# Performance work log

Measured on AMD Instinct MI355X. Metric: run time of the kernel, lower is better.

The kernel has to match this reference:

```python
import jax, jax.numpy as jnp
import numpy as np
import math

IN_C, OUT_C, KH, KW = 128, 128, 3, 3
GROUPS_NUM, NUM_W = 8, 8
STRIDE, PAD, DIL = 1, 1, 1
BETA = 1.0


def setup_inputs() -> dict:
    key = jax.random.key(0)
    ks = jax.random.split(key, 6)
    B, H, W = 8, 56, 56
    n = IN_C * KH * KW
    bound = math.sqrt(6.0 / n)  # reset_parameters bound for weight templates
    inputs = jax.random.normal(ks[0], (B, IN_C, H, W), jnp.float32)
    mask = jax.random.randint(ks[1], (B, H, W), 0, GROUPS_NUM)
    Alpha = jax.random.uniform(ks[2], (B, GROUPS_NUM, H, W), jnp.float32)
    weight_templates = jax.random.uniform(ks[3], (OUT_C * IN_C * KH * KW, NUM_W), jnp.float32, -bound, bound)
    routing_w = jax.random.normal(ks[4], (GROUPS_NUM * NUM_W, IN_C), jnp.float32) * 0.01
    routing_b = jnp.zeros((GROUPS_NUM * NUM_W,), jnp.float32)
    bias = jnp.zeros((OUT_C,), jnp.float32)
    return dict(inputs=inputs, mask=mask, Alpha=Alpha, weight_templates=weight_templates,
                routing_w=routing_w, routing_b=routing_b, bias=bias, use_alpha=1)


def _unfold(x):
    # torch F.unfold-compatible im2col: [B, C*KH*KW, Ho, Wo], channel-major feature order
    return jax.lax.conv_general_dilated_patches(
        x, (KH, KW), (STRIDE, STRIDE), [(PAD, PAD), (PAD, PAD)],
        rhs_dilation=(DIL, DIL), dimension_numbers=('NCHW', 'OIHW', 'NCHW'))


def reference(inputs, mask, Alpha, weight_templates, routing_w, routing_b, bias, use_alpha):
    B, C, H, W = inputs.shape
    K = IN_C * KH * KW
    # SE-style routing: GAP -> fc -> scaled sigmoid (alpha=1.0 in source)
    x_se = inputs.reshape(B, C, -1).mean(-1)                              # [B, C]
    x_se = 2.0 * jax.nn.sigmoid(x_se @ routing_w.T + routing_b) / NUM_W   # [B, G*num_W]
    # blend weight templates: F.linear(x_se.reshape(-1,num_W), weight)
    w = x_se.reshape(B * GROUPS_NUM, NUM_W) @ weight_templates.T          # [B*G, O*K]
    w = w.reshape(B, GROUPS_NUM, OUT_C, K).transpose(0, 2, 3, 1)          # [B, O, K, G]
    patches = _unfold(inputs)                                             # [B, K, Ho, Wo]
    # per-group convolution outputs, then per-pixel group routing
    y = jnp.einsum('bokg,bkhw->boghw', w, patches)                        # [B, O, G, Ho, Wo]
    if use_alpha:
        probs = jax.nn.softmax(BETA * Alpha, axis=1)                      # soft routing [B, G, Ho, Wo]
    else:
        probs = jax.nn.one_hot(mask, GROUPS_NUM, axis=1, dtype=y.dtype)   # hard per-pixel group select
    out = jnp.einsum('boghw,bghw->bohw', y, probs)
    return out + bias.reshape(1, -1, 1, 1)
```

## Files before the change

### kernel.cpp

```cpp
#include <hip/hip_runtime.h>
#include <stdint.h>

#define IN_C   128
#define OUT_C  128
#define KTOT   1152
#define NG     8
#define NW     8
#define NB     8
#define HH     56
#define WWID   56
#define NPIX   3136
#define PPAD   3200
#define MTOT   1024
#define HALO   58
#define HPIX   (HALO*HALO)


typedef __attribute__((ext_vector_type(8))) short short8;
typedef __attribute__((ext_vector_type(8))) unsigned short ushort8;
typedef __attribute__((ext_vector_type(4))) float f32x4;

__device__ __forceinline__ unsigned short f2bf(float f) {
    unsigned u = __float_as_uint(f);
    u += 0x7FFF + ((u >> 16) & 1);
    return (unsigned short)(u >> 16);
}

__device__ __forceinline__ void cp16(const unsigned short* g, unsigned short* l) {
    __builtin_amdgcn_global_load_lds(
        (const __attribute__((address_space(1))) unsigned int*)g,
        (__attribute__((address_space(3))) unsigned int*)l,
        16, 0, 0);
}

__global__ __launch_bounds__(256) void prep_kernel(const float* __restrict__ in,
                                                   const float* __restrict__ T,
                                                   float* __restrict__ xse,
                                                   unsigned short* __restrict__ Apack,
                                                   unsigned short* __restrict__ Xt) {
    __shared__ __align__(16) unsigned char smem[32768];
    const int blk = blockIdx.x;
    const int t = threadIdx.x;

    if (blk < 1024) {
        const float* src = in + (size_t)blk * NPIX;
        float s = 0.f;
        for (int i = t; i < NPIX / 4; i += 256) {
            float4 v = ((const float4*)src)[i];
            s += v.x + v.y + v.z + v.w;
        }
        #pragma unroll
        for (int off = 32; off; off >>= 1) s += __shfl_down(s, off);
        float* ws4 = (float*)smem;
        if ((t & 63) == 0) ws4[t >> 6] = s;
        __syncthreads();
        if (t == 0)
            xse[blk] = (ws4[0] + ws4[1] + ws4[2] + ws4[3]) * (1.0f / (float)NPIX);
        return;
    }
    if (blk < 1152) {
        unsigned short* lh = (unsigned short*)smem;
        const int o = blk - 1024;
        const float* To = T + (size_t)o * 9216;
        #pragma unroll
        for (int it = 0; it < 9; it++) {
            const int f = it * 256 + t;
            const float4 v = ((const float4*)To)[f];
            ushort4 h;
            h.x = f2bf(v.x); h.y = f2bf(v.y); h.z = f2bf(v.z); h.w = f2bf(v.w);
            *(ushort4*)&lh[f * 4] = h;
        }
        __syncthreads();
        const int m16b = o >> 1;
        const int lrb = (o & 1) * 8;
        #pragma unroll
        for (int it = 0; it < 5; it++) {
            const int ch = it * 256 + t;
            if (ch < 1152) {
                const int j = ch & 7, kc = ch >> 3;
                const int s = kc >> 4, c0 = (kc & 15) << 3;
                const int kt = kc >> 2, lq = kc & 3;
                ushort8 v;
                #pragma unroll
                for (int i = 0; i < 8; i++)
                    v[i] = lh[((c0 + i) * 9 + s) * 8 + j];
                const size_t off = ((((size_t)m16b * 36 + kt) * 4 + lq) * 16 + lrb + j) * 8;
                *(ushort8*)&Apack[off] = v;
            }
        }
        return;
    }
    unsigned short* tile = (unsigned short*)smem;
    const int idx = blk - 1152;
    const int yt = idx % 28;
    const int b  = idx / 28;
    const int y0 = yt * 2;

    #pragma unroll
    for (int it = 0; it < 14; it++) {
        const int f = it * 256 + t;
        const int c = f / 28;
        const int rem = f - c * 28;
        const int y = rem / 14;
        const int x4 = rem - y * 14;
        const float4 v = *(const float4*)(in + ((size_t)(b * IN_C + c)) * NPIX
                                          + (y0 + y) * WWID + x4 * 4);
        unsigned short bf0 = f2bf(v.x), bf1 = f2bf(v.y), bf2 = f2bf(v.z), bf3 = f2bf(v.w);
        const int ppb = (y * WWID + x4 * 4) ^ (((c >> 3) & 15) << 2);
        uint2 pk;
        pk.x = (unsigned)bf0 | ((unsigned)bf1 << 16);
        pk.y = (unsigned)bf2 | ((unsigned)bf3 << 16);
        *(uint2*)&tile[c * 128 + ppb] = pk;
    }
    __syncthreads();

    #pragma unroll
    for (int it = 0; it < 7; it++) {
        const int ch = it * 256 + t;
        const int oct = ch & 15;
        const int pp = ch >> 4;
        const int sw = oct << 2;
        ushort8 v;
        #pragma unroll
        for (int i = 0; i < 8; i++)
            v[i] = tile[(oct * 8 + i) * 128 + (pp ^ sw)];
        const int y2 = (pp >= WWID) ? 1 : 0;
        const int xg = pp - y2 * WWID;
        const size_t hp = (size_t)b * HPIX + (y0 + y2 + 1) * HALO + (xg + 1);
        *(ushort8*)&Xt[hp * 128 + oct * 8] = v;
    }

    if (t < 64) {
        const int pi = t >> 4, oct = t & 15;
        const int yy = y0 + 1 + (pi >> 1);
        const int xx = (pi & 1) * 57;
        *(ushort8*)&Xt[((size_t)b * HPIX + yy * HALO + xx) * 128 + oct * 8] =
            (ushort8){0, 0, 0, 0, 0, 0, 0, 0};
    }
    if (yt == 0 || yt == 27) {
        const int yy = (yt == 0) ? 0 : 57;
        #pragma unroll
        for (int it = 0; it < 4; it++) {
            const int ch = it * 256 + t;
            if (ch < 928) {
                const int xx = ch >> 4, oct = ch & 15;
                *(ushort8*)&Xt[((size_t)b * HPIX + yy * HALO + xx) * 128 + oct * 8] =
                    (ushort8){0, 0, 0, 0, 0, 0, 0, 0};
            }
        }
    }
}

__global__ __launch_bounds__(256) void s_kernel(const float* __restrict__ Alpha,
                                                const int* __restrict__ mask,
                                                const float* __restrict__ xse,
                                                const float* __restrict__ rw,
                                                const float* __restrict__ rb,
                                                const int* __restrict__ use_alpha,
                                                float* __restrict__ Sws) {
    const int b = blockIdx.y;
    const int t = threadIdx.x;
    const int p = blockIdx.x * 256 + t;
    __shared__ float xs[IN_C];
    __shared__ float rsh[64];
    if (t < IN_C) xs[t] = xse[b * IN_C + t];
    __syncthreads();
    if (t < 64) {
        float acc = rb[t];
        #pragma unroll 8
        for (int c = 0; c < IN_C; c++) acc += xs[c] * rw[t * IN_C + c];
        rsh[t] = 0.25f / (1.0f + expf(-acc));
    }
    __syncthreads();
    if (p >= PPAD) return;
    float sj[8] = {0, 0, 0, 0, 0, 0, 0, 0};
    if (p < NPIX) {
        float pr[8];
        if (use_alpha[0]) {
            float a[8], m = -1e30f;
            #pragma unroll
            for (int g = 0; g < 8; g++) {
                a[g] = Alpha[((size_t)(b * NG + g)) * NPIX + p];
                m = fmaxf(m, a[g]);
            }
            float sum = 0.f;
            #pragma unroll
            for (int g = 0; g < 8; g++) { pr[g] = expf(a[g] - m); sum += pr[g]; }
            float inv = 1.f / sum;
            #pragma unroll
            for (int g = 0; g < 8; g++) pr[g] *= inv;
        } else {
            int mg = mask[(size_t)b * NPIX + p];
            #pragma unroll
            for (int g = 0; g < 8; g++) pr[g] = (g == mg) ? 1.f : 0.f;
        }
        #pragma unroll
        for (int g = 0; g < 8; g++)
            #pragma unroll
            for (int j = 0; j < 8; j++) sj[j] += pr[g] * rsh[g * 8 + j];
    }
    float* dst = Sws + ((size_t)b * PPAD + p) * 8;
    *(f32x4*)dst = (f32x4){sj[0], sj[1], sj[2], sj[3]};
    *(f32x4*)(dst + 4) = (f32x4){sj[4], sj[5], sj[6], sj[7]};
}

__global__ __launch_bounds__(256) void gemm_kernel(const unsigned short* __restrict__ Apack,
                                                   const unsigned short* __restrict__ Xt,
                                                   const float* __restrict__ Sws,
                                                   const float* __restrict__ bias,
                                                   float* __restrict__ out) {
    __shared__ __align__(16) unsigned short Bsh[4][512 * 8];
    const int tid = threadIdx.x;
    const int wv = tid >> 6, ln = tid & 63;
    const int lq = ln >> 4, lr = ln & 15;
    const int wrow = wv >> 1, wcol = wv & 1;

    const int lid = blockIdx.x;
    const int b   = lid & 7;
    const int sl  = lid >> 3;
    const int mt  = sl & 7;
    const int nt  = sl >> 3;

    f32x4 acc[4][4];
    #pragma unroll
    for (int i = 0; i < 4; i++)
        #pragma unroll
        for (int j = 0; j < 4; j++) acc[i][j] = (f32x4){0.f, 0.f, 0.f, 0.f};

    const int js = tid & 3;
    const int r0 = tid >> 2,  q0 = js ^ (r0 & 3) ^ ((r0 >> 2) & 3);
    const int r1 = r0 + 64,   q1 = js ^ (r1 & 3) ^ ((r1 >> 2) & 3);
    const int p0 = min(nt * 128 + r0, NPIX - 1);
    const int p1 = min(nt * 128 + r1, NPIX - 1);
    const int y0p = p0 / WWID, x0p = p0 - y0p * WWID;
    const int y1p = p1 / WWID, x1p = p1 - y1p * WWID;
    const unsigned short* gb0 = Xt + ((size_t)b * HPIX + y0p * HALO + x0p) * 128 + q0 * 8;
    const unsigned short* gb1 = Xt + ((size_t)b * HPIX + y1p * HALO + x1p) * 128 + q1 * 8;
    unsigned short* lbA[4];
    #pragma unroll
    for (int i = 0; i < 4; i++) lbA[i] = &Bsh[i][(wv * 64) * 8];

    const unsigned short* gaw[4];
    #pragma unroll
    for (int tm = 0; tm < 4; tm++) {
        const int m16 = mt * 8 + wrow * 4 + tm;
        gaw[tm] = Apack + ((size_t)m16 * 36 * 64 + ln) * 8;
    }

    const int jj = lq ^ (lr & 3) ^ ((lr >> 2) & 3);

    cp16(gb0, lbA[0]); cp16(gb1, lbA[0] + 256 * 8);
    cp16(gb0 + 32, lbA[1]); cp16(gb1 + 32, lbA[1] + 256 * 8);
    short8 af[2][4];
    #pragma unroll
    for (int tm = 0; tm < 4; tm++) af[0][tm] = *(const short8*)(gaw[tm]);
    #pragma unroll
    for (int tm = 0; tm < 4; tm++) af[1][tm] = *(const short8*)(gaw[tm] + 512);

    #pragma unroll 1
    for (int pr = 0; pr < 18; pr++) {
        __syncthreads();
        const int st2 = pr * 2 + 2, st3 = pr * 2 + 3;
        if (pr < 17) {
            const int nk2 = st2 * 32, s2 = nk2 >> 7;
            const int kh2 = s2 / 3, kw2 = s2 - 3 * kh2;
            const int off2 = (kh2 * HALO + kw2) * 128 + (nk2 & 127);
            const int nk3 = st3 * 32, s3 = nk3 >> 7;
            const int kh3 = s3 / 3, kw3 = s3 - 3 * kh3;
            const int off3 = (kh3 * HALO + kw3) * 128 + (nk3 & 127);
            unsigned short* d2 = lbA[st2 & 3];
            unsigned short* d3 = lbA[st3 & 3];
            cp16(gb0 + off2, d2); cp16(gb1 + off2, d2 + 256 * 8);
            cp16(gb0 + off3, d3); cp16(gb1 + off3, d3 + 256 * 8);
        }
        const int bufa = (pr & 1) * 2;
        {
            short8 bfr[4];
            #pragma unroll
            for (int tn = 0; tn < 4; tn++) {
                const int row = wcol * 64 + tn * 16 + lr;
                bfr[tn] = *(const short8*)&Bsh[bufa][(row * 4 + jj) * 8];
            }
            #pragma unroll
            for (int tm = 0; tm < 4; tm++)
                #pragma unroll
                for (int tn = 0; tn < 4; tn++)
                    acc[tm][tn] = __builtin_amdgcn_mfma_f32_16x16x32_bf16(
                        af[0][tm], bfr[tn], acc[tm][tn], 0, 0, 0);
        }
        if (pr < 17) {
            #pragma unroll
            for (int tm = 0; tm < 4; tm++)
                af[0][tm] = *(const short8*)(gaw[tm] + (size_t)st2 * 512);
        }
        {
            short8 bfr[4];
            #pragma unroll
            for (int tn = 0; tn < 4; tn++) {
                const int row = wcol * 64 + tn * 16 + lr;
                bfr[tn] = *(const short8*)&Bsh[bufa + 1][(row * 4 + jj) * 8];
            }
            #pragma unroll
            for (int tm = 0; tm < 4; tm++)
                #pragma unroll
                for (int tn = 0; tn < 4; tn++)
                    acc[tm][tn] = __builtin_amdgcn_mfma_f32_16x16x32_bf16(
                        af[1][tm], bfr[tn], acc[tm][tn], 0, 0, 0);
        }
        if (pr < 17) {
            #pragma unroll
            for (int tm = 0; tm < 4; tm++)
                af[1][tm] = *(const short8*)(gaw[tm] + (size_t)st3 * 512);
        }
    }

    const int j0 = (lq & 1) * 4;
    const int oo = lq >> 1;
    #pragma unroll
    for (int tm = 0; tm < 4; tm++) {
        const int o = mt * 16 + wrow * 8 + tm * 2 + oo;
        const float bo = bias[o];
        #pragma unroll
        for (int tn = 0; tn < 4; tn++) {
            const int p = nt * 128 + wcol * 64 + tn * 16 + lr;
            const f32x4 sv = *(const f32x4*)&Sws[((size_t)b * PPAD + p) * 8 + j0];
            const f32x4 a = acc[tm][tn];
            float part = a.x * sv.x + a.y * sv.y + a.z * sv.z + a.w * sv.w;
            float tot = part + __shfl_xor(part, 16);
            if ((lq & 1) == 0 && p < NPIX)
                out[((size_t)b * OUT_C + o) * NPIX + p] = tot + bo;
        }
    }
}

extern "C" void kernel_launch(void* const* d_in, const int* in_sizes, int n_in,
                              void* d_out, int out_size, void* d_ws, size_t ws_size,
                              hipStream_t stream) {
    const float* inputs = (const float*)d_in[0];
    const int*   mask   = (const int*)d_in[1];
    const float* Alpha  = (const float*)d_in[2];
    const float* wtmpl  = (const float*)d_in[3];
    const float* rw     = (const float*)d_in[4];
    const float* rb     = (const float*)d_in[5];
    const float* bias   = (const float*)d_in[6];
    const int*   ua     = (const int*)d_in[7];
    float* out = (float*)d_out;

    char* ws = (char*)d_ws;
    unsigned short* Xt  = (unsigned short*)ws;
    unsigned short* Apk = (unsigned short*)(ws + 6889472);
    float*          Sws = (float*)(ws + 9248768);
    float*          xse = (float*)(ws + 10067968);

    prep_kernel<<<1376, 256, 0, stream>>>(inputs, wtmpl, xse, Apk, Xt);
    s_kernel<<<dim3(13, NB), 256, 0, stream>>>(Alpha, mask, xse, rw, rb, ua, Sws);
    gemm_kernel<<<1600, 256, 0, stream>>>(Apk, Xt, Sws, bias, out);
}
```

Baseline: 162.8 us.

## Interleave async LDS copies with MFMA clusters using barriers and priority

```diff
diff --git a/kernel.cpp b/kernel.cpp
--- a/kernel.cpp
+++ b/kernel.cpp
@@ -248,70 +248,107 @@
     }
 
     const int jj = lq ^ (lr & 3) ^ ((lr >> 2) & 3);
+    const int rowb = wcol * 64 + lr;
 
     cp16(gb0, lbA[0]); cp16(gb1, lbA[0] + 256 * 8);
     cp16(gb0 + 32, lbA[1]); cp16(gb1 + 32, lbA[1] + 256 * 8);
+    __builtin_amdgcn_sched_barrier(0);
     short8 af[2][4];
     #pragma unroll
     for (int tm = 0; tm < 4; tm++) af[0][tm] = *(const short8*)(gaw[tm]);
     #pragma unroll
     for (int tm = 0; tm < 4; tm++) af[1][tm] = *(const short8*)(gaw[tm] + 512);
+    __builtin_amdgcn_sched_barrier(0);
 
     #pragma unroll 1
     for (int pr = 0; pr < 18; pr++) {
-        __syncthreads();
         const int st2 = pr * 2 + 2, st3 = pr * 2 + 3;
-        if (pr < 17) {
-            const int nk2 = st2 * 32, s2 = nk2 >> 7;
-            const int kh2 = s2 / 3, kw2 = s2 - 3 * kh2;
-            const int off2 = (kh2 * HALO + kw2) * 128 + (nk2 & 127);
-            const int nk3 = st3 * 32, s3 = nk3 >> 7;
-            const int kh3 = s3 / 3, kw3 = s3 - 3 * kh3;
-            const int off3 = (kh3 * HALO + kw3) * 128 + (nk3 & 127);
-            unsigned short* d2 = lbA[st2 & 3];
-            unsigned short* d3 = lbA[st3 & 3];
-            cp16(gb0 + off2, d2); cp16(gb1 + off2, d2 + 256 * 8);
-            cp16(gb0 + off3, d3); cp16(gb1 + off3, d3 + 256 * 8);
-        }
         const int bufa = (pr & 1) * 2;
+        const int nk2 = st2 * 32, s2 = nk2 >> 7;
+        const int kh2 = s2 / 3, kw2 = s2 - 3 * kh2;
+        const int off2 = (kh2 * HALO + kw2) * 128 + (nk2 & 127);
+        const int nk3 = st3 * 32, s3 = nk3 >> 7;
+        const int kh3 = s3 / 3, kw3 = s3 - 3 * kh3;
+        const int off3 = (kh3 * HALO + kw3) * 128 + (nk3 & 127);
+        unsigned short* d2 = lbA[st2 & 3];
+        unsigned short* d3 = lbA[st3 & 3];
+
+        asm volatile("s_waitcnt vmcnt(4)" ::: "memory");
+        __builtin_amdgcn_sched_barrier(0);
+        __builtin_amdgcn_s_barrier();
+
+        if (pr < 17) cp16(gb0 + off2, d2);
+        __builtin_amdgcn_sched_barrier(0);
         {
-            short8 bfr[4];
-            #pragma unroll
-            for (int tn = 0; tn < 4; tn++) {
-                const int row = wcol * 64 + tn * 16 + lr;
-                bfr[tn] = *(const short8*)&Bsh[bufa][(row * 4 + jj) * 8];
-            }
-            #pragma unroll
-            for (int tm = 0; tm < 4; tm++)
-                #pragma unroll
-                for (int tn = 0; tn < 4; tn++)
-                    acc[tm][tn] = __builtin_amdgcn_mfma_f32_16x16x32_bf16(
-                        af[0][tm], bfr[tn], acc[tm][tn], 0, 0, 0);
-        }
+            short8 bf0 = *(const short8*)&Bsh[bufa][((rowb +  0) * 4 + jj) * 8];
+            short8 bf1 = *(const short8*)&Bsh[bufa][((rowb + 16) * 4 + jj) * 8];
+            __builtin_amdgcn_s_barrier();
+            __builtin_amdgcn_s_setprio(1);
+            #pragma unroll
+            for (int tm = 0; tm < 4; tm++) {
+                acc[tm][0] = __builtin_amdgcn_mfma_f32_16x16x32_bf16(af[0][tm], bf0, acc[tm][0], 0, 0, 0);
+                acc[tm][1] = __builtin_amdgcn_mfma_f32_16x16x32_bf16(af[0][tm], bf1, acc[tm][1], 0, 0, 0);
+            }
+            __builtin_amdgcn_s_setprio(0);
+            __builtin_amdgcn_s_barrier();
+        }
+
+        if (pr < 17) cp16(gb1 + off2, d2 + 256 * 8);
+        __builtin_amdgcn_sched_barrier(0);
+        {
+            short8 bf2 = *(const short8*)&Bsh[bufa][((rowb + 32) * 4 + jj) * 8];
+            short8 bf3 = *(const short8*)&Bsh[bufa][((rowb + 48) * 4 + jj) * 8];
+            __builtin_amdgcn_s_barrier();
+            __builtin_amdgcn_s_setprio(1);
+            #pragma unroll
+            for (int tm = 0; tm < 4; tm++) {
+                acc[tm][2] = __builtin_amdgcn_mfma_f32_16x16x32_bf16(af[0][tm], bf2, acc[tm][2], 0, 0, 0);
+                acc[tm][3] = __builtin_amdgcn_mfma_f32_16x16x32_bf16(af[0][tm], bf3, acc[tm][3], 0, 0, 0);
+            }
+            __builtin_amdgcn_s_setprio(0);
+            __builtin_amdgcn_s_barrier();
+        }
+
         if (pr < 17) {
             #pragma unroll
             for (int tm = 0; tm < 4; tm++)
                 af[0][tm] = *(const short8*)(gaw[tm] + (size_t)st2 * 512);
-        }
+            cp16(gb0 + off3, d3);
+            cp16(gb1 + off3, d3 + 256 * 8);
+        }
+        __builtin_amdgcn_sched_barrier(0);
         {
-            short8 bfr[4];
-            #pragma unroll
-            for (int tn = 0; tn < 4; tn++) {
-                const int row = wcol * 64 + tn * 16 + lr;
-                bfr[tn] = *(const short8*)&Bsh[bufa + 1][(row * 4 + jj) * 8];
-            }
-            #pragma unroll
-            for (int tm = 0; tm < 4; tm++)
-                #pragma unroll
-                for (int tn = 0; tn < 4; tn++)
-                    acc[tm][tn] = __builtin_amdgcn_mfma_f32_16x16x32_bf16(
-                        af[1][tm], bfr[tn], acc[tm][tn], 0, 0, 0);
+            short8 bf0 = *(const short8*)&Bsh[bufa + 1][((rowb +  0) * 4 + jj) * 8];
+            short8 bf1 = *(const short8*)&Bsh[bufa + 1][((rowb + 16) * 4 + jj) * 8];
+            __builtin_amdgcn_s_barrier();
+            __builtin_amdgcn_s_setprio(1);
+            #pragma unroll
+            for (int tm = 0; tm < 4; tm++) {
+                acc[tm][0] = __builtin_amdgcn_mfma_f32_16x16x32_bf16(af[1][tm], bf0, acc[tm][0], 0, 0, 0);
+                acc[tm][1] = __builtin_amdgcn_mfma_f32_16x16x32_bf16(af[1][tm], bf1, acc[tm][1], 0, 0, 0);
+            }
+            __builtin_amdgcn_s_setprio(0);
+            __builtin_amdgcn_s_barrier();
+        }
+
+        {
+            short8 bf2 = *(const short8*)&Bsh[bufa + 1][((rowb + 32) * 4 + jj) * 8];
+            short8 bf3 = *(const short8*)&Bsh[bufa + 1][((rowb + 48) * 4 + jj) * 8];
+            __builtin_amdgcn_s_barrier();
+            __builtin_amdgcn_s_setprio(1);
+            #pragma unroll
+            for (int tm = 0; tm < 4; tm++) {
+                acc[tm][2] = __builtin_amdgcn_mfma_f32_16x16x32_bf16(af[1][tm], bf2, acc[tm][2], 0, 0, 0);
+                acc[tm][3] = __builtin_amdgcn_mfma_f32_16x16x32_bf16(af[1][tm], bf3, acc[tm][3], 0, 0, 0);
+            }
+            __builtin_amdgcn_s_setprio(0);
         }
         if (pr < 17) {
             #pragma unroll
             for (int tm = 0; tm < 4; tm++)
                 af[1][tm] = *(const short8*)(gaw[tm] + (size_t)st3 * 512);
         }
+        __builtin_amdgcn_sched_barrier(0);
     }
 
     const int j0 = (lq & 1) * 4;
```

New measurement: 178.1 us. 9.4% more time.

## Load B fragments directly from global into registers, drop LDS staging and barriers

Applied to the files above, without the earlier changes.

```diff
diff --git a/kernel.cpp b/kernel.cpp
--- a/kernel.cpp
+++ b/kernel.cpp
@@ -209,7 +209,6 @@
                                                    const float* __restrict__ Sws,
                                                    const float* __restrict__ bias,
                                                    float* __restrict__ out) {
-    __shared__ __align__(16) unsigned short Bsh[4][512 * 8];
     const int tid = threadIdx.x;
     const int wv = tid >> 6, ln = tid & 63;
     const int lq = ln >> 4, lr = ln & 15;
@@ -227,92 +226,57 @@
         #pragma unroll
         for (int j = 0; j < 4; j++) acc[i][j] = (f32x4){0.f, 0.f, 0.f, 0.f};
 
-    const int js = tid & 3;
-    const int r0 = tid >> 2,  q0 = js ^ (r0 & 3) ^ ((r0 >> 2) & 3);
-    const int r1 = r0 + 64,   q1 = js ^ (r1 & 3) ^ ((r1 >> 2) & 3);
-    const int p0 = min(nt * 128 + r0, NPIX - 1);
-    const int p1 = min(nt * 128 + r1, NPIX - 1);
-    const int y0p = p0 / WWID, x0p = p0 - y0p * WWID;
-    const int y1p = p1 / WWID, x1p = p1 - y1p * WWID;
-    const unsigned short* gb0 = Xt + ((size_t)b * HPIX + y0p * HALO + x0p) * 128 + q0 * 8;
-    const unsigned short* gb1 = Xt + ((size_t)b * HPIX + y1p * HALO + x1p) * 128 + q1 * 8;
-    unsigned short* lbA[4];
-    #pragma unroll
-    for (int i = 0; i < 4; i++) lbA[i] = &Bsh[i][(wv * 64) * 8];
-
-    const unsigned short* gaw[4];
+    int aoff[4];
     #pragma unroll
     for (int tm = 0; tm < 4; tm++) {
         const int m16 = mt * 8 + wrow * 4 + tm;
-        gaw[tm] = Apack + ((size_t)m16 * 36 * 64 + ln) * 8;
-    }
-
-    const int jj = lq ^ (lr & 3) ^ ((lr >> 2) & 3);
-
-    cp16(gb0, lbA[0]); cp16(gb1, lbA[0] + 256 * 8);
-    cp16(gb0 + 32, lbA[1]); cp16(gb1 + 32, lbA[1] + 256 * 8);
-    short8 af[2][4];
-    #pragma unroll
-    for (int tm = 0; tm < 4; tm++) af[0][tm] = *(const short8*)(gaw[tm]);
-    #pragma unroll
-    for (int tm = 0; tm < 4; tm++) af[1][tm] = *(const short8*)(gaw[tm] + 512);
+        aoff[tm] = m16 * 18432 + ln * 8;
+    }
+    int boff[4];
+    #pragma unroll
+    for (int tn = 0; tn < 4; tn++) {
+        const int p = min(nt * 128 + wcol * 64 + tn * 16 + lr, NPIX - 1);
+        const int y = p / WWID, x = p - y * WWID;
+        boff[tn] = (y * HALO + x) * 128 + lq * 8;
+    }
+    const unsigned short* XtB = Xt + (size_t)b * HPIX * 128;
+
+#define LOADST(Ad, Bd, st_) {                                              \
+        const int s_ = (st_) >> 2;                                         \
+        const int kh_ = s_ / 3, kw_ = s_ - 3 * kh_;                        \
+        const int sB_ = (kh_ * HALO + kw_) * 128 + ((st_) & 3) * 32;       \
+        const int sA_ = (st_) * 512;                                       \
+        _Pragma("unroll")                                                  \
+        for (int tm_ = 0; tm_ < 4; tm_++)                                  \
+            Ad[tm_] = *(const short8*)(Apack + sA_ + aoff[tm_]);           \
+        _Pragma("unroll")                                                  \
+        for (int tn_ = 0; tn_ < 4; tn_++)                                  \
+            Bd[tn_] = *(const short8*)(XtB + sB_ + boff[tn_]);             \
+    }
+
+    short8 A0[4], B0[4], A1[4], B1[4];
+    LOADST(A0, B0, 0);
+    LOADST(A1, B1, 1);
 
     #pragma unroll 1
-    for (int pr = 0; pr < 18; pr++) {
-        __syncthreads();
-        const int st2 = pr * 2 + 2, st3 = pr * 2 + 3;
-        if (pr < 17) {
-            const int nk2 = st2 * 32, s2 = nk2 >> 7;
-            const int kh2 = s2 / 3, kw2 = s2 - 3 * kh2;
-            const int off2 = (kh2 * HALO + kw2) * 128 + (nk2 & 127);
-            const int nk3 = st3 * 32, s3 = nk3 >> 7;
-            const int kh3 = s3 / 3, kw3 = s3 - 3 * kh3;
-            const int off3 = (kh3 * HALO + kw3) * 128 + (nk3 & 127);
-            unsigned short* d2 = lbA[st2 & 3];
-            unsigned short* d3 = lbA[st3 & 3];
-            cp16(gb0 + off2, d2); cp16(gb1 + off2, d2 + 256 * 8);
-            cp16(gb0 + off3, d3); cp16(gb1 + off3, d3 + 256 * 8);
-        }
-        const int bufa = (pr & 1) * 2;
-        {
-            short8 bfr[4];
-            #pragma unroll
-            for (int tn = 0; tn < 4; tn++) {
-                const int row = wcol * 64 + tn * 16 + lr;
-                bfr[tn] = *(const short8*)&Bsh[bufa][(row * 4 + jj) * 8];
-            }
-            #pragma unroll
-            for (int tm = 0; tm < 4; tm++)
-                #pragma unroll
-                for (int tn = 0; tn < 4; tn++)
-                    acc[tm][tn] = __builtin_amdgcn_mfma_f32_16x16x32_bf16(
-                        af[0][tm], bfr[tn], acc[tm][tn], 0, 0, 0);
-        }
-        if (pr < 17) {
-            #pragma unroll
-            for (int tm = 0; tm < 4; tm++)
-                af[0][tm] = *(const short8*)(gaw[tm] + (size_t)st2 * 512);
-        }
-        {
-            short8 bfr[4];
-            #pragma unroll
-            for (int tn = 0; tn < 4; tn++) {
-                const int row = wcol * 64 + tn * 16 + lr;
-                bfr[tn] = *(const short8*)&Bsh[bufa + 1][(row * 4 + jj) * 8];
-            }
-            #pragma unroll
-            for (int tm = 0; tm < 4; tm++)
-                #pragma unroll
-                for (int tn = 0; tn < 4; tn++)
-                    acc[tm][tn] = __builtin_amdgcn_mfma_f32_16x16x32_bf16(
-                        af[1][tm], bfr[tn], acc[tm][tn], 0, 0, 0);
-        }
-        if (pr < 17) {
-            #pragma unroll
-            for (int tm = 0; tm < 4; tm++)
-                af[1][tm] = *(const short8*)(gaw[tm] + (size_t)st3 * 512);
-        }
-    }
+    for (int it = 0; it < 18; it++) {
+        const int st2 = it * 2 + 2, st3 = it * 2 + 3;
+        #pragma unroll
+        for (int tm = 0; tm < 4; tm++)
+            #pragma unroll
+            for (int tn = 0; tn < 4; tn++)
+                acc[tm][tn] = __builtin_amdgcn_mfma_f32_16x16x32_bf16(
+                    A0[tm], B0[tn], acc[tm][tn], 0, 0, 0);
+        if (it < 17) LOADST(A0, B0, st2);
+        #pragma unroll
+        for (int tm = 0; tm < 4; tm++)
+            #pragma unroll
+            for (int tn = 0; tn < 4; tn++)
+                acc[tm][tn] = __builtin_amdgcn_mfma_f32_16x16x32_bf16(
+                    A1[tm], B1[tn], acc[tm][tn], 0, 0, 0);
+        if (it < 17) LOADST(A1, B1, st3);
+    }
+#undef LOADST
 
     const int j0 = (lq & 1) * 4;
     const int oo = lq >> 1;
```

Result: slower. 235.3 us (+44.5%).
